# Kernel optimization log

Measured on AMD Instinct MI355X. Metric: run time of the kernel, lower is better.

## Reference

```python
import jax, jax.numpy as jnp
import numpy as np
import math

D = 256      # d_model == channels
H = 8        # nhead
DEP = D // H # depth = 32
FF = 1024    # dim_feedforward
P = 81       # 9x9 shogi board tokens
EPS = 1e-5


def setup_inputs() -> dict:
    key = jax.random.key(0)
    ks = jax.random.split(key, 8)
    B = 2048
    x = jax.random.normal(ks[0], (B, D, 9, 9), dtype=jnp.float32)
    s = 0.02
    return {
        "x": x,
        "qkv_w": jax.random.normal(ks[1], (3 * D, D // H), dtype=jnp.float32) * s,  # grouped 1x1 conv weight
        "rel_w1": jax.random.normal(ks[2], (32, D * P), dtype=jnp.float32) * s,
        "rel_w2": jax.random.normal(ks[3], (DEP * P, 32), dtype=jnp.float32) * s,
        "o_w": jax.random.normal(ks[4], (D, D), dtype=jnp.float32) * s,
        "ff_w1": jax.random.normal(ks[5], (FF, D), dtype=jnp.float32) * s,
        "ff_w2": jax.random.normal(ks[6], (D, FF), dtype=jnp.float32) * s,
        "bn1_g": jnp.ones((D,), jnp.float32),
        "bn1_b": jnp.zeros((D,), jnp.float32),
        "bn2_g": jnp.ones((D,), jnp.float32),
        "bn2_b": jnp.zeros((D,), jnp.float32),
    }


def _batchnorm(x, g, b):
    # training-mode BN: per-channel batch stats over (B, H, W), biased variance
    mean = jnp.mean(x, axis=(0, 2, 3), keepdims=True)
    var = jnp.var(x, axis=(0, 2, 3), keepdims=True)
    return (x - mean) * jax.lax.rsqrt(var + EPS) * g[None, :, None, None] + b[None, :, None, None]


def reference(x, qkv_w, rel_w1, rel_w2, o_w, ff_w1, ff_w2, bn1_g, bn1_b, bn2_g, bn2_b):
    B = x.shape[0]
    # grouped 1x1 conv QKV: group g maps its D//H input channels to 3*DEP outputs
    xg = x.reshape(B, H, D // H, P)                      # [B, H, D/H, 81]
    wg = qkv_w.reshape(H, 3 * DEP, D // H)               # [H, 3*DEP, D/H]
    qkv = jnp.einsum('goi,bgip->bgop', wg, xg).reshape(B, 3 * D, P)
    q = qkv[:, :D].reshape(B, H, DEP, P).transpose(0, 1, 3, 2)       # [B,H,81,DEP]
    k = qkv[:, D:2 * D].reshape(B, H, DEP, P)                        # [B,H,DEP,81]
    v = qkv[:, 2 * D:].reshape(B, H, DEP, P).transpose(0, 1, 3, 2)   # [B,H,81,DEP]
    # learned relative-position bias from the whole board state
    r = (x.reshape(B, -1) @ rel_w1.T) @ rel_w2.T          # [B, DEP*81]
    r = r.reshape(B, 1, DEP, P)                           # broadcast over heads
    scores = (q @ k + q @ r) / math.sqrt(DEP)             # [B,H,81,81]
    aw = jax.nn.softmax(scores, axis=-1)
    att = (aw @ v).transpose(0, 1, 3, 2).reshape(B, D, 9, 9)
    att = jnp.einsum('oc,bchw->bohw', o_w, att)           # 1x1 output projection
    x1 = _batchnorm(att + x, bn1_g, bn1_b)
    ff = jax.nn.gelu(jnp.einsum('fc,bchw->bfhw', ff_w1, x1), approximate=False)
    ff = jnp.einsum('cf,bfhw->bchw', ff_w2, ff)
    return _batchnorm(ff + x1, bn2_g, bn2_b)
```

## Files before the change

kernel.cpp:

```cpp
#include <hip/hip_runtime.h>
#include <math.h>

#define B_   2048
#define D_   256
#define H_   8
#define DEP_ 32
#define P_   81
#define FF_  1024
#define CHW  (D_*P_)
#define NPOS (B_*P_)
#define KREL (D_*P_)
#define NTOT (B_*CHW)
#define EPS_ 1e-5f
#define YTP  264
#define YTSZ (96*YTP)

typedef __attribute__((ext_vector_type(8))) short short8v;
typedef __attribute__((ext_vector_type(4))) short short4v;
typedef __attribute__((ext_vector_type(4))) float f32x4;

__device__ __forceinline__ float bf2f(unsigned short u){
    return __uint_as_float(((unsigned int)u) << 16);
}
__device__ __forceinline__ unsigned short f2bf(float f){
    unsigned int x = __float_as_uint(f);
    return (unsigned short)((x + 0x7FFFu + ((x >> 16) & 1u)) >> 16);
}
__device__ __forceinline__ float fast_gelu(float x){
    float s = __builtin_amdgcn_rcpf(1.f + __expf(-1.702f * x));
    return x * s;
}
__device__ __forceinline__ float wave16_red(float v){
    v += __shfl_xor(v, 1); v += __shfl_xor(v, 2);
    v += __shfl_xor(v, 4); v += __shfl_xor(v, 8);
    return v;
}
__device__ __forceinline__ short8v frag_redist(const f32x4 c0, const f32x4 c1, int lr, int lh){
    short8v o;
    #pragma unroll
    for (int j = 0; j < 8; ++j){
        int src = lr + 16 * (2 * (lh & 1) + (j >> 2));
        float v0 = __shfl(c0[j & 3], src);
        float v1 = __shfl(c1[j & 3], src);
        o[j] = (short)f2bf(lh < 2 ? v0 : v1);
    }
    return o;
}

__global__ __launch_bounds__(256) void k_prep(const float* __restrict__ relw1,
                                              const float* __restrict__ ffw2,
                                              const float* __restrict__ qkvw,
                                              const float* __restrict__ ow,
                                              unsigned short* __restrict__ w1rel,
                                              unsigned short* __restrict__ w2bf,
                                              unsigned short* __restrict__ qkvwb,
                                              unsigned short* __restrict__ owb){
    int i = blockIdx.x * 256 + threadIdx.x;
    int st = gridDim.x * 256;
    for (; i < 1015808; i += st){
        if (i < 663552)                w1rel[i]           = f2bf(relw1[i]);
        else if (i < 925696)           w2bf[i - 663552]   = f2bf(ffw2[i - 663552]);
        else if (i < 950272)           qkvwb[i - 925696]  = f2bf(qkvw[i - 925696]);
        else                           owb[i - 950272]    = f2bf(ow[i - 950272]);
    }
}

__global__ __launch_bounds__(256) void k_h_mfma(const float* __restrict__ x,
                                                const unsigned short* __restrict__ w1b,
                                                float* __restrict__ ph){
    const int bt = blockIdx.x >> 2, ks = blockIdx.x & 3;
    const int t = threadIdx.x, w = t >> 6, lane = t & 63;
    const int lr = lane & 15, lh = lane >> 4;
    const int b0 = bt * 16;
    f32x4 acc0 = {0.f,0.f,0.f,0.f}, acc1 = {0.f,0.f,0.f,0.f};
    const float* xrow = x + (size_t)(b0 + lr) * KREL;
    const unsigned short* wr0 = w1b + (size_t)lr * KREL;
    const unsigned short* wr1 = w1b + (size_t)(16 + lr) * KREL;
    for (int kk = w; kk < 162; kk += 4){
        const int k0 = (ks * 162 + kk) * 32 + lh * 8;
        short8v a0 = *(const short8v*)(wr0 + k0);
        short8v a1 = *(const short8v*)(wr1 + k0);
        const float4 xv0 = *(const float4*)(xrow + k0);
        const float4 xv1 = *(const float4*)(xrow + k0 + 4);
        short8v bb;
        bb[0] = (short)f2bf(xv0.x); bb[1] = (short)f2bf(xv0.y);
        bb[2] = (short)f2bf(xv0.z); bb[3] = (short)f2bf(xv0.w);
        bb[4] = (short)f2bf(xv1.x); bb[5] = (short)f2bf(xv1.y);
        bb[6] = (short)f2bf(xv1.z); bb[7] = (short)f2bf(xv1.w);
        acc0 = __builtin_amdgcn_mfma_f32_16x16x32_bf16(a0, bb, acc0, 0, 0, 0);
        acc1 = __builtin_amdgcn_mfma_f32_16x16x32_bf16(a1, bb, acc1, 0, 0, 0);
    }
    __shared__ float red[4][32][17];
    #pragma unroll
    for (int r = 0; r < 4; ++r){
        red[w][lh * 4 + r][lr]      = acc0[r];
        red[w][16 + lh * 4 + r][lr] = acc1[r];
    }
    __syncthreads();
    for (int i = t; i < 512; i += 256){
        int j = i >> 4, bb2 = i & 15;
        float s = red[0][j][bb2] + red[1][j][bb2] + red[2][j][bb2] + red[3][j][bb2];
        ph[(size_t)ks * 65536 + (size_t)(b0 + bb2) * 32 + j] = s;
    }
}

__global__ __launch_bounds__(256) void k_h_red(const float* __restrict__ ph,
                                               float* __restrict__ h){
    int i = blockIdx.x * 256 + threadIdx.x;
    h[i] = ph[i] + ph[65536 + i] + ph[131072 + i] + ph[196608 + i];
}

__global__ __launch_bounds__(512, 2) void k_attn_oproj8(const float* __restrict__ x,
                                                        const unsigned short* __restrict__ qkvwb,
                                                        const float* __restrict__ relw2,
                                                        const float* __restrict__ h,
                                                        const unsigned short* __restrict__ owb,
                                                        unsigned short* __restrict__ yT,
                                                        float* __restrict__ p1){
    const int b = blockIdx.x, t = threadIdx.x;
    const int lane = t & 63, w = t >> 6;
    const int lr = lane & 15, lh = lane >> 4;

    __shared__ __align__(16) unsigned short x1s[96 * 264];
    __shared__ __align__(16) unsigned short Rl[96 * 40];
    __shared__ __align__(16) unsigned short vL[8][32 * 104];
    __shared__ __align__(16) unsigned short pL[8][16 * 104];
    unsigned short* attT = (unsigned short*)vL;

    const float* xb = x + (size_t)b * CHW;

    {
        const float* hb = h + b * 32;
        float hreg[32];
        #pragma unroll
        for (int j = 0; j < 32; ++j) hreg[j] = hb[j];
        for (int idx = t; idx < 2592; idx += 512){
            int d = idx / 81, p = idx - d * 81;
            const float4* wr = (const float4*)(relw2 + (size_t)idx * 32);
            float s = 0.f;
            #pragma unroll
            for (int j = 0; j < 8; ++j){
                float4 wv = wr[j];
                s += wv.x * hreg[4*j] + wv.y * hreg[4*j+1] + wv.z * hreg[4*j+2] + wv.w * hreg[4*j+3];
            }
            Rl[p * 40 + d] = f2bf(s);
        }
        for (int idx = t; idx < 15 * 32; idx += 512){
            int p = 81 + (idx >> 5), d = idx & 31;
            Rl[p * 40 + d] = 0;
        }
    }
    for (int idx = t; idx < 15 * 132; idx += 512){
        int r = idx / 132, c = idx - r * 132;
        *(unsigned int*)&x1s[(81 + r) * 264 + 2 * c] = 0;
    }
    for (int idx = t; idx < 81 * 128; idx += 512){
        int c2 = idx / 81, p = idx - c2 * 81;
        int c = 2 * c2;
        unsigned int pk = (unsigned int)f2bf(xb[c * 81 + p])
                        | ((unsigned int)f2bf(xb[(c + 1) * 81 + p]) << 16);
        *(unsigned int*)&x1s[p * 264 + c] = pk;
    }
    __syncthreads();

    const int hh = w;
    const int qrow = hh * 32, krow = 256 + hh * 32, vrow = 512 + hh * 32;
    const int gq = (qrow / 96) * 32, gk = (krow / 96) * 32, gv = (vrow / 96) * 32;
    unsigned short* v_ = vL[w];
    unsigned short* p_ = pL[w];

    __builtin_amdgcn_s_setprio(1);
    short8v bqf[6];
    {
        short8v a0 = *(const short8v*)(qkvwb + (size_t)(qrow + lr) * 32 + lh * 8);
        short8v a1 = *(const short8v*)(qkvwb + (size_t)(qrow + 16 + lr) * 32 + lh * 8);
        #pragma unroll
        for (int nt = 0; nt < 6; ++nt){
            short8v bb = *(const short8v*)(x1s + (nt * 16 + lr) * 264 + gq + lh * 8);
            f32x4 c0 = {0.f,0.f,0.f,0.f}, c1 = {0.f,0.f,0.f,0.f};
            c0 = __builtin_amdgcn_mfma_f32_16x16x32_bf16(a0, bb, c0, 0, 0, 0);
            c1 = __builtin_amdgcn_mfma_f32_16x16x32_bf16(a1, bb, c1, 0, 0, 0);
            bqf[nt] = frag_redist(c0, c1, lr, lh);
        }
    }
    short8v akf[6];
    {
        short8v a0 = *(const short8v*)(qkvwb + (size_t)(krow + lr) * 32 + lh * 8);
        short8v a1 = *(const short8v*)(qkvwb + (size_t)(krow + 16 + lr) * 32 + lh * 8);
        #pragma unroll
        for (int mt = 0; mt < 6; ++mt){
            int p = mt * 16 + lr;
            short4v r0 = *(const short4v*)(Rl + p * 40 + lh * 4);
            short4v r1 = *(const short4v*)(Rl + p * 40 + 16 + lh * 4);
            f32x4 c0, c1;
            #pragma unroll
            for (int r = 0; r < 4; ++r){
                c0[r] = bf2f((unsigned short)r0[r]);
                c1[r] = bf2f((unsigned short)r1[r]);
            }
            short8v bb = *(const short8v*)(x1s + p * 264 + gk + lh * 8);
            c0 = __builtin_amdgcn_mfma_f32_16x16x32_bf16(a0, bb, c0, 0, 0, 0);
            c1 = __builtin_amdgcn_mfma_f32_16x16x32_bf16(a1, bb, c1, 0, 0, 0);
            akf[mt] = frag_redist(c0, c1, lr, lh);
        }
    }
    {
        short8v a0 = *(const short8v*)(qkvwb + (size_t)(vrow + lr) * 32 + lh * 8);
        short8v a1 = *(const short8v*)(qkvwb + (size_t)(vrow + 16 + lr) * 32 + lh * 8);
        #pragma unroll
        for (int nt = 0; nt < 6; ++nt){
            short8v bb = *(const short8v*)(x1s + (nt * 16 + lr) * 264 + gv + lh * 8);
            f32x4 c0 = {0.f,0.f,0.f,0.f}, c1 = {0.f,0.f,0.f,0.f};
            c0 = __builtin_amdgcn_mfma_f32_16x16x32_bf16(a0, bb, c0, 0, 0, 0);
            c1 = __builtin_amdgcn_mfma_f32_16x16x32_bf16(a1, bb, c1, 0, 0, 0);
            int pk = nt * 16 + lr;
            #pragma unroll
            for (int r = 0; r < 4; ++r){
                v_[(lh * 4 + r) * 104 + pk]      = f2bf(c0[r]);
                v_[(16 + lh * 4 + r) * 104 + pk] = f2bf(c1[r]);
            }
        }
    }

    f32x4 oA[6], oB[6];
    #pragma unroll
    for (int nt = 0; nt < 6; ++nt){
        f32x4 sc[6];
        #pragma unroll
        for (int mt = 0; mt < 6; ++mt){
            f32x4 z = {0.f,0.f,0.f,0.f};
            sc[mt] = __builtin_amdgcn_mfma_f32_16x16x32_bf16(akf[mt], bqf[nt], z, 0, 0, 0);
        }
        sc[5][0] = (lh == 0) ? sc[5][0] : -1e30f;
        sc[5][1] = -1e30f; sc[5][2] = -1e30f; sc[5][3] = -1e30f;
        float mx = -1e30f;
        #pragma unroll
        for (int mt = 0; mt < 6; ++mt)
        #pragma unroll
        for (int r = 0; r < 4; ++r) mx = fmaxf(mx, sc[mt][r]);
        mx = fmaxf(mx, __shfl_xor(mx, 16));
        mx = fmaxf(mx, __shfl_xor(mx, 32));
        const float scl = 0.17677669529663687f;
        float sum = 0.f;
        #pragma unroll
        for (int mt = 0; mt < 6; ++mt)
        #pragma unroll
        for (int r = 0; r < 4; ++r){
            float e = __expf((sc[mt][r] - mx) * scl);
            sc[mt][r] = e; sum += e;
        }
        sum += __shfl_xor(sum, 16);
        sum += __shfl_xor(sum, 32);
        float inv = 1.f / sum;
        #pragma unroll
        for (int mt = 0; mt < 6; ++mt){
            short4v pv;
            #pragma unroll
            for (int r = 0; r < 4; ++r) pv[r] = (short)f2bf(sc[mt][r] * inv);
            *(short4v*)(p_ + lr * 104 + mt * 16 + lh * 4) = pv;
        }
        f32x4 o0 = {0.f,0.f,0.f,0.f}, o1 = {0.f,0.f,0.f,0.f};
        #pragma unroll
        for (int ks = 0; ks < 3; ++ks){
            short8v ap  = *(const short8v*)(p_ + lr * 104 + ks * 32 + lh * 8);
            short8v bv0 = *(const short8v*)(v_ + lr * 104 + ks * 32 + lh * 8);
            short8v bv1 = *(const short8v*)(v_ + (16 + lr) * 104 + ks * 32 + lh * 8);
            o0 = __builtin_amdgcn_mfma_f32_16x16x32_bf16(ap, bv0, o0, 0, 0, 0);
            o1 = __builtin_amdgcn_mfma_f32_16x16x32_bf16(ap, bv1, o1, 0, 0, 0);
        }
        oA[nt] = o0;
        oB[nt] = o1;
    }
    __builtin_amdgcn_s_setprio(0);

    __syncthreads();
    #pragma unroll
    for (int nt = 0; nt < 6; ++nt){
        #pragma unroll
        for (int r = 0; r < 4; ++r){
            int pq = nt * 16 + lh * 4 + r;
            if (pq < 81){
                attT[pq * 264 + hh * 32 + lr]      = f2bf(oA[nt][r]);
                attT[pq * 264 + hh * 32 + 16 + lr] = f2bf(oB[nt][r]);
            } else {
                attT[pq * 264 + hh * 32 + lr]      = 0;
                attT[pq * 264 + hh * 32 + 16 + lr] = 0;
            }
        }
    }
    __syncthreads();

    const int cw = w * 32;
    f32x4 acc[2][6];
    #pragma unroll
    for (int ci = 0; ci < 2; ++ci)
    #pragma unroll
    for (int pj = 0; pj < 6; ++pj)
        acc[ci][pj] = (f32x4){0.f, 0.f, 0.f, 0.f};

    __builtin_amdgcn_s_setprio(1);
    for (int ks = 0; ks < 8; ++ks){
        const int k0 = ks * 32 + lh * 8;
        short8v a[2];
        #pragma unroll
        for (int ci = 0; ci < 2; ++ci)
            a[ci] = *(const short8v*)(owb + (size_t)(cw + ci * 16 + lr) * 256 + k0);
        #pragma unroll
        for (int pj = 0; pj < 6; ++pj){
            short8v bb = *(const short8v*)(attT + (pj * 16 + lr) * 264 + k0);
            #pragma unroll
            for (int ci = 0; ci < 2; ++ci)
                acc[ci][pj] = __builtin_amdgcn_mfma_f32_16x16x32_bf16(a[ci], bb, acc[ci][pj], 0, 0, 0);
        }
    }
    __builtin_amdgcn_s_setprio(0);
    unsigned short* yb = yT + (size_t)b * YTSZ;
    float cs[8], cq[8];
    #pragma unroll
    for (int i = 0; i < 8; ++i){ cs[i] = 0.f; cq[i] = 0.f; }
    #pragma unroll
    for (int ci = 0; ci < 2; ++ci)
    #pragma unroll
    for (int pj = 0; pj < 6; ++pj){
        int p = pj * 16 + lr;
        int c = cw + ci * 16 + lh * 4;
        short4v pk;
        if (p < 81){
            short4v xv = *(const short4v*)&x1s[p * 264 + c];
            #pragma unroll
            for (int r = 0; r < 4; ++r){
                float y = acc[ci][pj][r] + bf2f((unsigned short)xv[r]);
                pk[r] = (short)f2bf(y);
                cs[ci * 4 + r] += y;
                cq[ci * 4 + r] += y * y;
            }
        } else {
            #pragma unroll
            for (int r = 0; r < 4; ++r) pk[r] = 0;
        }
        *(short4v*)(yb + p * YTP + c) = pk;
    }
    #pragma unroll
    for (int i = 0; i < 8; ++i){
        cs[i] = wave16_red(cs[i]);
        cq[i] = wave16_red(cq[i]);
    }
    if (lr == 0){
        #pragma unroll
        for (int ci = 0; ci < 2; ++ci)
        #pragma unroll
        for (int r = 0; r < 4; ++r){
            int c = cw + ci * 16 + lh * 4 + r;
            p1[(size_t)c * 2048 + b]         = cs[ci * 4 + r];
            p1[(size_t)(256 + c) * 2048 + b] = cq[ci * 4 + r];
        }
    }
}

__global__ __launch_bounds__(256) void k_red(const float* __restrict__ part,
                                             const float* __restrict__ g, const float* __restrict__ bia,
                                             float* __restrict__ sOut, float* __restrict__ tOut){
    const int c = blockIdx.x, t = threadIdx.x;
    float s = 0.f, q = 0.f;
    #pragma unroll
    for (int i = 0; i < 8; ++i){
        s += part[(size_t)c * 2048 + t + i * 256];
        q += part[(size_t)(256 + c) * 2048 + t + i * 256];
    }
    __shared__ float rs[256], rq[256];
    rs[t] = s; rq[t] = q;
    __syncthreads();
    for (int k = 128; k; k >>= 1){
        if (t < k){ rs[t] += rs[t + k]; rq[t] += rq[t + k]; }
        __syncthreads();
    }
    if (t == 0){
        float m = rs[0] / (float)NPOS;
        float var = rq[0] / (float)NPOS - m * m;
        float sc = g[c] * rsqrtf(var + EPS_);
        sOut[c] = sc;
        tOut[c] = bia[c] - m * sc;
    }
}

__global__ __launch_bounds__(256) void k_w1prep(const float* __restrict__ w1,
                                                const float* __restrict__ s1v,
                                                const float* __restrict__ t1v,
                                                unsigned short* __restrict__ w1s,
                                                float* __restrict__ bias1){
    const int f = blockIdx.x, t = threadIdx.x;
    float wv = w1[f * 256 + t];
    w1s[f * 256 + t] = f2bf(wv * s1v[t]);
    float s = wv * t1v[t];
    #pragma unroll
    for (int m = 1; m < 64; m <<= 1) s += __shfl_xor(s, m);
    __shared__ float red[4];
    if ((t & 63) == 0) red[t >> 6] = s;
    __syncthreads();
    if (t == 0) bias1[f] = red[0] + red[1] + red[2] + red[3];
}

__global__ __launch_bounds__(256, 2) void k_ff_v4(unsigned short* __restrict__ yT,
                                                  const unsigned short* __restrict__ w1s,
                                                  const unsigned short* __restrict__ w2bf,
                                                  const float* __restrict__ bias1,
                                                  const float* __restrict__ s1, const float* __restrict__ t1,
                                                  float* __restrict__ p2){
    const int b = blockIdx.x, t = threadIdx.x;
    const int lane = t & 63, w = t >> 6;
    const int lr = lane & 15, lh = lane >> 4;

    __shared__ __align__(16) unsigned short x1s[96 * 264];
    __shared__ __align__(16) unsigned short ffs[2][96 * 72];

    {
        const short8v* src = (const short8v*)(yT + (size_t)b * YTSZ);
        short8v* dst = (short8v*)x1s;
        for (int idx = t; idx < 3168; idx += 256) dst[idx] = src[idx];
    }
    __syncthreads();

    const int cw = w * 64;
    const int fl = w * 16 + lh * 4;
    f32x4 acc2[4][6];
    #pragma unroll
    for (int ci = 0; ci < 4; ++ci)
    #pragma unroll
    for (int pj = 0; pj < 6; ++pj)
        acc2[ci][pj] = (f32x4){0.f, 0.f, 0.f, 0.f};

    auto g1_kloop = [&](int fc, f32x4 (&acc1)[6]){
        const int fbase = fc * 64 + w * 16;
        float b4[4];
        #pragma unroll
        for (int r = 0; r < 4; ++r) b4[r] = bias1[fbase + lh * 4 + r];
        #pragma unroll
        for (int pj = 0; pj < 6; ++pj){
            acc1[pj][0] = b4[0]; acc1[pj][1] = b4[1];
            acc1[pj][2] = b4[2]; acc1[pj][3] = b4[3];
        }
        __builtin_amdgcn_s_setprio(1);
        #pragma unroll
        for (int ks = 0; ks < 8; ++ks){
            const int k0 = ks * 32 + lh * 8;
            short8v a0 = *(const short8v*)(w1s + (size_t)(fbase + lr) * 256 + k0);
            #pragma unroll
            for (int pj = 0; pj < 6; ++pj){
                short8v bb = *(const short8v*)(x1s + (pj * 16 + lr) * 264 + k0);
                acc1[pj] = __builtin_amdgcn_mfma_f32_16x16x32_bf16(a0, bb, acc1[pj], 0, 0, 0);
            }
        }
        __builtin_amdgcn_s_setprio(0);
    };
    auto g2 = [&](int fc, int bf){
        __builtin_amdgcn_s_setprio(1);
        #pragma unroll
        for (int ks2 = 0; ks2 < 2; ++ks2){
            const int k0 = ks2 * 32 + lh * 8;
            short8v a2[4];
            #pragma unroll
            for (int ci = 0; ci < 4; ++ci)
                a2[ci] = *(const short8v*)(w2bf + (size_t)(cw + ci * 16 + lr) * 1024 + fc * 64 + k0);
            #pragma unroll
            for (int pj = 0; pj < 6; ++pj){
                short8v bb = *(const short8v*)(ffs[bf] + (pj * 16 + lr) * 72 + k0);
                #pragma unroll
                for (int ci = 0; ci < 4; ++ci)
                    acc2[ci][pj] = __builtin_amdgcn_mfma_f32_16x16x32_bf16(a2[ci], bb, acc2[ci][pj], 0, 0, 0);
            }
        }
        __builtin_amdgcn_s_setprio(0);
    };
    auto gelu_store = [&](const f32x4 (&acc1)[6], int bf){
        #pragma unroll
        for (int pj = 0; pj < 6; ++pj){
            int p = pj * 16 + lr;
            short4v pk;
            #pragma unroll
            for (int r = 0; r < 4; ++r)
                pk[r] = (short)f2bf(fast_gelu(acc1[pj][r]));
            *(short4v*)&ffs[bf][p * 72 + fl] = pk;
        }
    };

    {
        f32x4 acc1[6];
        g1_kloop(0, acc1);
        gelu_store(acc1, 0);
    }
    __syncthreads();
    for (int fc = 0; fc < 15; ++fc){
        f32x4 acc1[6];
        g1_kloop(fc + 1, acc1);
        g2(fc, fc & 1);
        gelu_store(acc1, (fc + 1) & 1);
        __syncthreads();
    }
    g2(15, 1);

    float sv[16], tv[16];
    #pragma unroll
    for (int ci = 0; ci < 4; ++ci)
    #pragma unroll
    for (int r = 0; r < 4; ++r){
        int c = cw + ci * 16 + lh * 4 + r;
        sv[ci * 4 + r] = s1[c];
        tv[ci * 4 + r] = t1[c];
    }
    unsigned short* zb = yT + (size_t)b * YTSZ;
    float cs[16], cq[16];
    #pragma unroll
    for (int i = 0; i < 16; ++i){ cs[i] = 0.f; cq[i] = 0.f; }
    #pragma unroll
    for (int ci = 0; ci < 4; ++ci)
    #pragma unroll
    for (int pj = 0; pj < 6; ++pj){
        int p = pj * 16 + lr;
        if (p < 81){
            int c = cw + ci * 16 + lh * 4;
            short4v yv = *(const short4v*)&x1s[p * 264 + c];
            short4v pk;
            #pragma unroll
            for (int r = 0; r < 4; ++r){
                float x1 = fmaf(bf2f((unsigned short)yv[r]), sv[ci * 4 + r], tv[ci * 4 + r]);
                float z = acc2[ci][pj][r] + x1;
                pk[r] = (short)f2bf(z);
                cs[ci * 4 + r] += z;
                cq[ci * 4 + r] += z * z;
            }
            *(short4v*)(zb + p * YTP + c) = pk;
        }
    }
    #pragma unroll
    for (int i = 0; i < 16; ++i){
        cs[i] = wave16_red(cs[i]);
        cq[i] = wave16_red(cq[i]);
    }
    if (lr == 0){
        #pragma unroll
        for (int ci = 0; ci < 4; ++ci)
        #pragma unroll
        for (int r = 0; r < 4; ++r){
            int c = cw + ci * 16 + lh * 4 + r;
            p2[(size_t)c * 2048 + b]         = cs[ci * 4 + r];
            p2[(size_t)(256 + c) * 2048 + b] = cq[ci * 4 + r];
        }
    }
}

__global__ __launch_bounds__(256) void k_bnapply_t(const unsigned short* __restrict__ yTz,
                                                   const float* __restrict__ s2, const float* __restrict__ t2,
                                                   float* __restrict__ out){
    const int b = blockIdx.x, t = threadIdx.x;
    __shared__ __align__(16) unsigned short zs[96 * 264];
    __shared__ float s2s[256], t2s[256];
    s2s[t] = s2[t];
    t2s[t] = t2[t];
    {
        const short8v* src = (const short8v*)(yTz + (size_t)b * YTSZ);
        short8v* dst = (short8v*)zs;
        for (int idx = t; idx < 3168; idx += 256) dst[idx] = src[idx];
    }
    __syncthreads();
    float* ob = out + (size_t)b * CHW;
    for (int idx = t; idx < CHW; idx += 256){
        int c = idx / 81, p = idx - c * 81;
        ob[idx] = fmaf(bf2f(zs[p * 264 + c]), s2s[c], t2s[c]);
    }
}

extern "C" void kernel_launch(void* const* d_in, const int* in_sizes, int n_in,
                              void* d_out, int out_size, void* d_ws, size_t ws_size,
                              hipStream_t stream){
    const float* x     = (const float*)d_in[0];
    const float* qkvw  = (const float*)d_in[1];
    const float* relw1 = (const float*)d_in[2];
    const float* relw2 = (const float*)d_in[3];
    const float* ow    = (const float*)d_in[4];
    const float* ffw1  = (const float*)d_in[5];
    const float* ffw2  = (const float*)d_in[6];
    const float* g1    = (const float*)d_in[7];
    const float* b1    = (const float*)d_in[8];
    const float* g2    = (const float*)d_in[9];
    const float* b2    = (const float*)d_in[10];
    float* out = (float*)d_out;
    char* ws = (char*)d_ws;

    unsigned short* w1rel = (unsigned short*)ws;
    float* h     = (float*)(ws + 1327104);
    unsigned short* w2bf  = (unsigned short*)(ws + 2117632);
    unsigned short* qkvwb = (unsigned short*)(ws + 2641920);
    unsigned short* owb   = (unsigned short*)(ws + 2691072);
    unsigned short* w1s   = (unsigned short*)(ws + 2822144);
    float* bias1 = (float*)(ws + 3346432);
    float* s1    = (float*)(ws + 3350528);
    float* t1    = (float*)(ws + 3351552);
    float* s2    = (float*)(ws + 3352576);
    float* t2    = (float*)(ws + 3353600);
    float* p1    = (float*)(ws + 3354624);
    float* p2    = (float*)(ws + 7548928);
    unsigned short* yT = (unsigned short*)(ws + 11743232);
    float* p_h = p1;

    hipLaunchKernelGGL(k_prep, dim3(1024), dim3(256), 0, stream,
                       relw1, ffw2, qkvw, ow, w1rel, w2bf, qkvwb, owb);
    hipLaunchKernelGGL(k_h_mfma, dim3(512), dim3(256), 0, stream, x, w1rel, p_h);
    hipLaunchKernelGGL(k_h_red,  dim3(256), dim3(256), 0, stream, p_h, h);
    hipLaunchKernelGGL(k_attn_oproj8, dim3(2048), dim3(512), 0, stream, x, qkvwb, relw2, h, owb, yT, p1);
    hipLaunchKernelGGL(k_red,     dim3(256),  dim3(256), 0, stream, p1, g1, b1, s1, t1);
    hipLaunchKernelGGL(k_w1prep,  dim3(1024), dim3(256), 0, stream, ffw1, s1, t1, w1s, bias1);
    hipLaunchKernelGGL(k_ff_v4,   dim3(2048), dim3(256), 0, stream, yT, w1s, w2bf, bias1, s1, t1, p2);
    hipLaunchKernelGGL(k_red,     dim3(256),  dim3(256), 0, stream, p2, g2, b2, s2, t2);
    hipLaunchKernelGGL(k_bnapply_t, dim3(2048), dim3(256), 0, stream, yT, s2, t2, out);
}
```

Before: 690.8 us.

## Switch FFN kernel to 32x32x16 MFMA tiles with larger F chunks

Rewrites the fused FFN kernel to use 32x32x16 bf16 MFMA instructions instead of 16x16x32, processing 128-wide F chunks (8 iterations instead of 16). The double-buffered software pipeline between GEMM1 and GEMM2 is replaced by a single buffer with two barriers per chunk. The intent is to cut instruction count and operand loads per FLOP and reduce the number of synchronisation rounds, at the cost of losing overlap between GELU/GEMM1 and GEMM2. Padding rows 81..95 are now computed in 32-row tiles, which adds wasted work.

```diff
diff --git a/kernel.cpp b/kernel.cpp
--- a/kernel.cpp
+++ b/kernel.cpp
@@ -18,6 +18,7 @@
 typedef __attribute__((ext_vector_type(8))) short short8v;
 typedef __attribute__((ext_vector_type(4))) short short4v;
 typedef __attribute__((ext_vector_type(4))) float f32x4;
+typedef __attribute__((ext_vector_type(16))) float f32x16;
 
 __device__ __forceinline__ float bf2f(unsigned short u){
     return __uint_as_float(((unsigned int)u) << 16);
@@ -33,6 +34,12 @@
 __device__ __forceinline__ float wave16_red(float v){
     v += __shfl_xor(v, 1); v += __shfl_xor(v, 2);
     v += __shfl_xor(v, 4); v += __shfl_xor(v, 8);
+    return v;
+}
+__device__ __forceinline__ float wave32_red(float v){
+    v += __shfl_xor(v, 1); v += __shfl_xor(v, 2);
+    v += __shfl_xor(v, 4); v += __shfl_xor(v, 8);
+    v += __shfl_xor(v, 16);
     return v;
 }
 __device__ __forceinline__ short8v frag_redist(const f32x4 c0, const f32x4 c1, int lr, int lh){
@@ -400,7 +407,7 @@
     if (t == 0) bias1[f] = red[0] + red[1] + red[2] + red[3];
 }
 
-__global__ __launch_bounds__(256, 2) void k_ff_v4(unsigned short* __restrict__ yT,
+__global__ __launch_bounds__(256, 2) void k_ff_v6(unsigned short* __restrict__ yT,
                                                   const unsigned short* __restrict__ w1s,
                                                   const unsigned short* __restrict__ w2bf,
                                                   const float* __restrict__ bias1,
@@ -408,10 +415,10 @@
                                                   float* __restrict__ p2){
     const int b = blockIdx.x, t = threadIdx.x;
     const int lane = t & 63, w = t >> 6;
-    const int lr = lane & 15, lh = lane >> 4;
+    const int lc = lane & 31, hi = lane >> 5;
 
     __shared__ __align__(16) unsigned short x1s[96 * 264];
-    __shared__ __align__(16) unsigned short ffs[2][96 * 72];
+    __shared__ __align__(16) unsigned short ffs[96 * 136];
 
     {
         const short8v* src = (const short8v*)(yT + (size_t)b * YTSZ);
@@ -421,129 +428,125 @@
     __syncthreads();
 
     const int cw = w * 64;
-    const int fl = w * 16 + lh * 4;
-    f32x4 acc2[4][6];
-    #pragma unroll
-    for (int ci = 0; ci < 4; ++ci)
-    #pragma unroll
-    for (int pj = 0; pj < 6; ++pj)
-        acc2[ci][pj] = (f32x4){0.f, 0.f, 0.f, 0.f};
-
-    auto g1_kloop = [&](int fc, f32x4 (&acc1)[6]){
-        const int fbase = fc * 64 + w * 16;
-        float b4[4];
-        #pragma unroll
-        for (int r = 0; r < 4; ++r) b4[r] = bias1[fbase + lh * 4 + r];
-        #pragma unroll
-        for (int pj = 0; pj < 6; ++pj){
-            acc1[pj][0] = b4[0]; acc1[pj][1] = b4[1];
-            acc1[pj][2] = b4[2]; acc1[pj][3] = b4[3];
+    f32x16 acc2[2][3];
+    #pragma unroll
+    for (int ct = 0; ct < 2; ++ct)
+    #pragma unroll
+    for (int pt = 0; pt < 3; ++pt)
+    #pragma unroll
+    for (int i = 0; i < 16; ++i)
+        acc2[ct][pt][i] = 0.f;
+
+    for (int fc = 0; fc < 8; ++fc){
+        const int fbase = fc * 128 + w * 32;
+        f32x16 acc1[3];
+        {
+            float bv[16];
+            #pragma unroll
+            for (int q = 0; q < 4; ++q)
+            #pragma unroll
+            for (int r = 0; r < 4; ++r)
+                bv[q * 4 + r] = bias1[fbase + 8 * q + 4 * hi + r];
+            #pragma unroll
+            for (int pt = 0; pt < 3; ++pt)
+            #pragma unroll
+            for (int i = 0; i < 16; ++i)
+                acc1[pt][i] = bv[i];
         }
         __builtin_amdgcn_s_setprio(1);
         #pragma unroll
+        for (int ks = 0; ks < 16; ++ks){
+            const int k0 = ks * 16 + hi * 8;
+            short8v a0 = *(const short8v*)(w1s + (size_t)(fbase + lc) * 256 + k0);
+            #pragma unroll
+            for (int pt = 0; pt < 3; ++pt){
+                short8v bb = *(const short8v*)(x1s + (pt * 32 + lc) * 264 + k0);
+                acc1[pt] = __builtin_amdgcn_mfma_f32_32x32x16_bf16(a0, bb, acc1[pt], 0, 0, 0);
+            }
+        }
+        __builtin_amdgcn_s_setprio(0);
+        #pragma unroll
+        for (int pt = 0; pt < 3; ++pt){
+            int p = pt * 32 + lc;
+            #pragma unroll
+            for (int q = 0; q < 4; ++q){
+                short4v pk;
+                #pragma unroll
+                for (int r = 0; r < 4; ++r)
+                    pk[r] = (short)f2bf(fast_gelu(acc1[pt][q * 4 + r]));
+                *(short4v*)&ffs[p * 136 + w * 32 + 8 * q + 4 * hi] = pk;
+            }
+        }
+        __syncthreads();
+        __builtin_amdgcn_s_setprio(1);
+        #pragma unroll
         for (int ks = 0; ks < 8; ++ks){
-            const int k0 = ks * 32 + lh * 8;
-            short8v a0 = *(const short8v*)(w1s + (size_t)(fbase + lr) * 256 + k0);
-            #pragma unroll
-            for (int pj = 0; pj < 6; ++pj){
-                short8v bb = *(const short8v*)(x1s + (pj * 16 + lr) * 264 + k0);
-                acc1[pj] = __builtin_amdgcn_mfma_f32_16x16x32_bf16(a0, bb, acc1[pj], 0, 0, 0);
+            const int kf = ks * 16 + hi * 8;
+            short8v a[2];
+            #pragma unroll
+            for (int ct = 0; ct < 2; ++ct)
+                a[ct] = *(const short8v*)(w2bf + (size_t)(cw + ct * 32 + lc) * 1024 + fc * 128 + kf);
+            #pragma unroll
+            for (int pt = 0; pt < 3; ++pt){
+                short8v bb = *(const short8v*)(ffs + (pt * 32 + lc) * 136 + kf);
+                #pragma unroll
+                for (int ct = 0; ct < 2; ++ct)
+                    acc2[ct][pt] = __builtin_amdgcn_mfma_f32_32x32x16_bf16(a[ct], bb, acc2[ct][pt], 0, 0, 0);
             }
         }
         __builtin_amdgcn_s_setprio(0);
-    };
-    auto g2 = [&](int fc, int bf){
-        __builtin_amdgcn_s_setprio(1);
-        #pragma unroll
-        for (int ks2 = 0; ks2 < 2; ++ks2){
-            const int k0 = ks2 * 32 + lh * 8;
-            short8v a2[4];
-            #pragma unroll
-            for (int ci = 0; ci < 4; ++ci)
-                a2[ci] = *(const short8v*)(w2bf + (size_t)(cw + ci * 16 + lr) * 1024 + fc * 64 + k0);
-            #pragma unroll
-            for (int pj = 0; pj < 6; ++pj){
-                short8v bb = *(const short8v*)(ffs[bf] + (pj * 16 + lr) * 72 + k0);
+        __syncthreads();
+    }
+    unsigned short* zb = yT + (size_t)b * YTSZ;
+    #pragma unroll
+    for (int ct = 0; ct < 2; ++ct){
+        float sv[16], tv[16];
+        #pragma unroll
+        for (int q = 0; q < 4; ++q)
+        #pragma unroll
+        for (int r = 0; r < 4; ++r){
+            int c = cw + ct * 32 + 8 * q + 4 * hi + r;
+            sv[q * 4 + r] = s1[c];
+            tv[q * 4 + r] = t1[c];
+        }
+        float cs[16], cq[16];
+        #pragma unroll
+        for (int i = 0; i < 16; ++i){ cs[i] = 0.f; cq[i] = 0.f; }
+        #pragma unroll
+        for (int pt = 0; pt < 3; ++pt){
+            int p = pt * 32 + lc;
+            if (p < 81){
                 #pragma unroll
-                for (int ci = 0; ci < 4; ++ci)
-                    acc2[ci][pj] = __builtin_amdgcn_mfma_f32_16x16x32_bf16(a2[ci], bb, acc2[ci][pj], 0, 0, 0);
-            }
-        }
-        __builtin_amdgcn_s_setprio(0);
-    };
-    auto gelu_store = [&](const f32x4 (&acc1)[6], int bf){
-        #pragma unroll
-        for (int pj = 0; pj < 6; ++pj){
-            int p = pj * 16 + lr;
-            short4v pk;
-            #pragma unroll
-            for (int r = 0; r < 4; ++r)
-                pk[r] = (short)f2bf(fast_gelu(acc1[pj][r]));
-            *(short4v*)&ffs[bf][p * 72 + fl] = pk;
-        }
-    };
-
-    {
-        f32x4 acc1[6];
-        g1_kloop(0, acc1);
-        gelu_store(acc1, 0);
-    }
-    __syncthreads();
-    for (int fc = 0; fc < 15; ++fc){
-        f32x4 acc1[6];
-        g1_kloop(fc + 1, acc1);
-        g2(fc, fc & 1);
-        gelu_store(acc1, (fc + 1) & 1);
-        __syncthreads();
-    }
-    g2(15, 1);
-
-    float sv[16], tv[16];
-    #pragma unroll
-    for (int ci = 0; ci < 4; ++ci)
-    #pragma unroll
-    for (int r = 0; r < 4; ++r){
-        int c = cw + ci * 16 + lh * 4 + r;
-        sv[ci * 4 + r] = s1[c];
-        tv[ci * 4 + r] = t1[c];
-    }
-    unsigned short* zb = yT + (size_t)b * YTSZ;
-    float cs[16], cq[16];
-    #pragma unroll
-    for (int i = 0; i < 16; ++i){ cs[i] = 0.f; cq[i] = 0.f; }
-    #pragma unroll
-    for (int ci = 0; ci < 4; ++ci)
-    #pragma unroll
-    for (int pj = 0; pj < 6; ++pj){
-        int p = pj * 16 + lr;
-        if (p < 81){
-            int c = cw + ci * 16 + lh * 4;
-            short4v yv = *(const short4v*)&x1s[p * 264 + c];
-            short4v pk;
+                for (int q = 0; q < 4; ++q){
+                    int c = cw + ct * 32 + 8 * q + 4 * hi;
+                    short4v yv = *(const short4v*)&x1s[p * 264 + c];
+                    short4v pk;
+                    #pragma unroll
+                    for (int r = 0; r < 4; ++r){
+                        float x1 = fmaf(bf2f((unsigned short)yv[r]), sv[q * 4 + r], tv[q * 4 + r]);
+                        float z = acc2[ct][pt][q * 4 + r] + x1;
+                        pk[r] = (short)f2bf(z);
+                        cs[q * 4 + r] += z;
+                        cq[q * 4 + r] += z * z;
+                    }
+                    *(short4v*)(zb + p * YTP + c) = pk;
+                }
+            }
+        }
+        #pragma unroll
+        for (int i = 0; i < 16; ++i){
+            cs[i] = wave32_red(cs[i]);
+            cq[i] = wave32_red(cq[i]);
+        }
+        if (lc == 0){
+            #pragma unroll
+            for (int q = 0; q < 4; ++q)
             #pragma unroll
             for (int r = 0; r < 4; ++r){
-                float x1 = fmaf(bf2f((unsigned short)yv[r]), sv[ci * 4 + r], tv[ci * 4 + r]);
-                float z = acc2[ci][pj][r] + x1;
-                pk[r] = (short)f2bf(z);
-                cs[ci * 4 + r] += z;
-                cq[ci * 4 + r] += z * z;
-            }
-            *(short4v*)(zb + p * YTP + c) = pk;
-        }
-    }
-    #pragma unroll
-    for (int i = 0; i < 16; ++i){
-        cs[i] = wave16_red(cs[i]);
-        cq[i] = wave16_red(cq[i]);
-    }
-    if (lr == 0){
-        #pragma unroll
-        for (int ci = 0; ci < 4; ++ci)
-        #pragma unroll
-        for (int r = 0; r < 4; ++r){
-            int c = cw + ci * 16 + lh * 4 + r;
-            p2[(size_t)c * 2048 + b]         = cs[ci * 4 + r];
-            p2[(size_t)(256 + c) * 2048 + b] = cq[ci * 4 + r];
+                int c = cw + ct * 32 + 8 * q + 4 * hi + r;
+                p2[(size_t)c * 2048 + b]         = cs[q * 4 + r];
+                p2[(size_t)(256 + c) * 2048 + b] = cq[q * 4 + r];
+            }
         }
     }
 }
@@ -609,7 +612,7 @@
     hipLaunchKernelGGL(k_attn_oproj8, dim3(2048), dim3(512), 0, stream, x, qkvwb, relw2, h, owb, yT, p1);
     hipLaunchKernelGGL(k_red,     dim3(256),  dim3(256), 0, stream, p1, g1, b1, s1, t1);
     hipLaunchKernelGGL(k_w1prep,  dim3(1024), dim3(256), 0, stream, ffw1, s1, t1, w1s, bias1);
-    hipLaunchKernelGGL(k_ff_v4,   dim3(2048), dim3(256), 0, stream, yT, w1s, w2bf, bias1, s1, t1, p2);
+    hipLaunchKernelGGL(k_ff_v6,   dim3(2048), dim3(256), 0, stream, yT, w1s, w2bf, bias1, s1, t1, p2);
     hipLaunchKernelGGL(k_red,     dim3(256),  dim3(256), 0, stream, p2, g2, b2, s2, t2);
     hipLaunchKernelGGL(k_bnapply_t, dim3(2048), dim3(256), 0, stream, yT, s2, t2, out);
 }
```

Result: slower. 704.7 us (+2.0%).

## Retile FF kernel waves as 2x2 over features and positions

Applied to the files above, without the earlier changes.

Splits the four waves of the feed-forward kernel into a 2x2 grid, with two halves over features/channels and two halves over positions, instead of each wave owning one feature/channel slice across all positions. Each wave now loads two W1 fragments per k-step and eight W2 fragments per chunk, and reuses each activation fragment across more MFMAs, which changes the balance of LDS reads to global weight reads. Because two position halves now produce partial BN statistics for the same channels, they are written to two buffers (reusing p1 as the second) and summed by a new k_red2. This raises accumulator register pressure (acc2 is 8x3), which may threaten the two-blocks-per-SIMD occupancy target.

```diff
diff --git a/kernel.cpp b/kernel.cpp
--- a/kernel.cpp
+++ b/kernel.cpp
@@ -383,6 +383,35 @@
     }
 }
 
+__global__ __launch_bounds__(256) void k_red2(const float* __restrict__ pa,
+                                              const float* __restrict__ pb,
+                                              const float* __restrict__ g, const float* __restrict__ bia,
+                                              float* __restrict__ sOut, float* __restrict__ tOut){
+    const int c = blockIdx.x, t = threadIdx.x;
+    float s = 0.f, q = 0.f;
+    #pragma unroll
+    for (int i = 0; i < 8; ++i){
+        size_t idx = (size_t)c * 2048 + t + i * 256;
+        size_t idq = (size_t)(256 + c) * 2048 + t + i * 256;
+        s += pa[idx] + pb[idx];
+        q += pa[idq] + pb[idq];
+    }
+    __shared__ float rs[256], rq[256];
+    rs[t] = s; rq[t] = q;
+    __syncthreads();
+    for (int k = 128; k; k >>= 1){
+        if (t < k){ rs[t] += rs[t + k]; rq[t] += rq[t + k]; }
+        __syncthreads();
+    }
+    if (t == 0){
+        float m = rs[0] / (float)NPOS;
+        float var = rq[0] / (float)NPOS - m * m;
+        float sc = g[c] * rsqrtf(var + EPS_);
+        sOut[c] = sc;
+        tOut[c] = bia[c] - m * sc;
+    }
+}
+
 __global__ __launch_bounds__(256) void k_w1prep(const float* __restrict__ w1,
                                                 const float* __restrict__ s1v,
                                                 const float* __restrict__ t1v,
@@ -400,15 +429,18 @@
     if (t == 0) bias1[f] = red[0] + red[1] + red[2] + red[3];
 }
 
-__global__ __launch_bounds__(256, 2) void k_ff_v4(unsigned short* __restrict__ yT,
+__global__ __launch_bounds__(256, 2) void k_ff_v9(unsigned short* __restrict__ yT,
                                                   const unsigned short* __restrict__ w1s,
                                                   const unsigned short* __restrict__ w2bf,
                                                   const float* __restrict__ bias1,
                                                   const float* __restrict__ s1, const float* __restrict__ t1,
-                                                  float* __restrict__ p2){
+                                                  float* __restrict__ p2a,
+                                                  float* __restrict__ p2b){
     const int b = blockIdx.x, t = threadIdx.x;
     const int lane = t & 63, w = t >> 6;
     const int lr = lane & 15, lh = lane >> 4;
+    const int wf = w & 1, wp = w >> 1;
+    const int p0 = wp * 48;
 
     __shared__ __align__(16) unsigned short x1s[96 * 264];
     __shared__ __align__(16) unsigned short ffs[2][96 * 72];
@@ -420,34 +452,39 @@
     }
     __syncthreads();
 
-    const int cw = w * 64;
-    const int fl = w * 16 + lh * 4;
-    f32x4 acc2[4][6];
-    #pragma unroll
-    for (int ci = 0; ci < 4; ++ci)
-    #pragma unroll
-    for (int pj = 0; pj < 6; ++pj)
+    f32x4 acc2[8][3];
+    #pragma unroll
+    for (int ci = 0; ci < 8; ++ci)
+    #pragma unroll
+    for (int pj = 0; pj < 3; ++pj)
         acc2[ci][pj] = (f32x4){0.f, 0.f, 0.f, 0.f};
 
-    auto g1_kloop = [&](int fc, f32x4 (&acc1)[6]){
-        const int fbase = fc * 64 + w * 16;
-        float b4[4];
-        #pragma unroll
-        for (int r = 0; r < 4; ++r) b4[r] = bias1[fbase + lh * 4 + r];
-        #pragma unroll
-        for (int pj = 0; pj < 6; ++pj){
-            acc1[pj][0] = b4[0]; acc1[pj][1] = b4[1];
-            acc1[pj][2] = b4[2]; acc1[pj][3] = b4[3];
+    auto g1_kloop = [&](int fc, f32x4 (&acc1)[2][3]){
+        const int fbase = fc * 64 + wf * 32;
+        float b4[2][4];
+        #pragma unroll
+        for (int fi = 0; fi < 2; ++fi)
+        #pragma unroll
+        for (int r = 0; r < 4; ++r)
+            b4[fi][r] = bias1[fbase + fi * 16 + lh * 4 + r];
+        #pragma unroll
+        for (int fi = 0; fi < 2; ++fi)
+        #pragma unroll
+        for (int pj = 0; pj < 3; ++pj){
+            acc1[fi][pj][0] = b4[fi][0]; acc1[fi][pj][1] = b4[fi][1];
+            acc1[fi][pj][2] = b4[fi][2]; acc1[fi][pj][3] = b4[fi][3];
         }
         __builtin_amdgcn_s_setprio(1);
         #pragma unroll
         for (int ks = 0; ks < 8; ++ks){
             const int k0 = ks * 32 + lh * 8;
             short8v a0 = *(const short8v*)(w1s + (size_t)(fbase + lr) * 256 + k0);
-            #pragma unroll
-            for (int pj = 0; pj < 6; ++pj){
-                short8v bb = *(const short8v*)(x1s + (pj * 16 + lr) * 264 + k0);
-                acc1[pj] = __builtin_amdgcn_mfma_f32_16x16x32_bf16(a0, bb, acc1[pj], 0, 0, 0);
+            short8v a1 = *(const short8v*)(w1s + (size_t)(fbase + 16 + lr) * 256 + k0);
+            #pragma unroll
+            for (int pj = 0; pj < 3; ++pj){
+                short8v bb = *(const short8v*)(x1s + (p0 + pj * 16 + lr) * 264 + k0);
+                acc1[0][pj] = __builtin_amdgcn_mfma_f32_16x16x32_bf16(a0, bb, acc1[0][pj], 0, 0, 0);
+                acc1[1][pj] = __builtin_amdgcn_mfma_f32_16x16x32_bf16(a1, bb, acc1[1][pj], 0, 0, 0);
             }
         }
         __builtin_amdgcn_s_setprio(0);
@@ -457,40 +494,43 @@
         #pragma unroll
         for (int ks2 = 0; ks2 < 2; ++ks2){
             const int k0 = ks2 * 32 + lh * 8;
-            short8v a2[4];
-            #pragma unroll
-            for (int ci = 0; ci < 4; ++ci)
-                a2[ci] = *(const short8v*)(w2bf + (size_t)(cw + ci * 16 + lr) * 1024 + fc * 64 + k0);
-            #pragma unroll
-            for (int pj = 0; pj < 6; ++pj){
-                short8v bb = *(const short8v*)(ffs[bf] + (pj * 16 + lr) * 72 + k0);
+            short8v a2[8];
+            #pragma unroll
+            for (int ci = 0; ci < 8; ++ci)
+                a2[ci] = *(const short8v*)(w2bf + (size_t)(wf * 128 + ci * 16 + lr) * 1024 + fc * 64 + k0);
+            #pragma unroll
+            for (int pj = 0; pj < 3; ++pj){
+                short8v bb = *(const short8v*)(ffs[bf] + (p0 + pj * 16 + lr) * 72 + k0);
                 #pragma unroll
-                for (int ci = 0; ci < 4; ++ci)
+                for (int ci = 0; ci < 8; ++ci)
                     acc2[ci][pj] = __builtin_amdgcn_mfma_f32_16x16x32_bf16(a2[ci], bb, acc2[ci][pj], 0, 0, 0);
             }
         }
         __builtin_amdgcn_s_setprio(0);
     };
-    auto gelu_store = [&](const f32x4 (&acc1)[6], int bf){
-        #pragma unroll
-        for (int pj = 0; pj < 6; ++pj){
-            int p = pj * 16 + lr;
+    auto gelu_store = [&](const f32x4 (&acc1)[2][3], int bf){
+        #pragma unroll
+        for (int fi = 0; fi < 2; ++fi)
+        #pragma unroll
+        for (int pj = 0; pj < 3; ++pj){
+            int p = p0 + pj * 16 + lr;
+            int fl = wf * 32 + fi * 16 + lh * 4;
             short4v pk;
             #pragma unroll
             for (int r = 0; r < 4; ++r)
-                pk[r] = (short)f2bf(fast_gelu(acc1[pj][r]));
+                pk[r] = (short)f2bf(fast_gelu(acc1[fi][pj][r]));
             *(short4v*)&ffs[bf][p * 72 + fl] = pk;
         }
     };
 
     {
-        f32x4 acc1[6];
+        f32x4 acc1[2][3];
         g1_kloop(0, acc1);
         gelu_store(acc1, 0);
     }
     __syncthreads();
     for (int fc = 0; fc < 15; ++fc){
-        f32x4 acc1[6];
+        f32x4 acc1[2][3];
         g1_kloop(fc + 1, acc1);
         g2(fc, fc & 1);
         gelu_store(acc1, (fc + 1) & 1);
@@ -498,52 +538,43 @@
     }
     g2(15, 1);
 
-    float sv[16], tv[16];
-    #pragma unroll
-    for (int ci = 0; ci < 4; ++ci)
-    #pragma unroll
-    for (int r = 0; r < 4; ++r){
-        int c = cw + ci * 16 + lh * 4 + r;
-        sv[ci * 4 + r] = s1[c];
-        tv[ci * 4 + r] = t1[c];
-    }
     unsigned short* zb = yT + (size_t)b * YTSZ;
-    float cs[16], cq[16];
-    #pragma unroll
-    for (int i = 0; i < 16; ++i){ cs[i] = 0.f; cq[i] = 0.f; }
-    #pragma unroll
-    for (int ci = 0; ci < 4; ++ci)
-    #pragma unroll
-    for (int pj = 0; pj < 6; ++pj){
-        int p = pj * 16 + lr;
-        if (p < 81){
-            int c = cw + ci * 16 + lh * 4;
-            short4v yv = *(const short4v*)&x1s[p * 264 + c];
-            short4v pk;
+    float* pout = wp ? p2b : p2a;
+    #pragma unroll
+    for (int ci = 0; ci < 8; ++ci){
+        const int c = wf * 128 + ci * 16 + lh * 4;
+        float sv4[4], tv4[4];
+        #pragma unroll
+        for (int r = 0; r < 4; ++r){ sv4[r] = s1[c + r]; tv4[r] = t1[c + r]; }
+        float cs4[4] = {0.f,0.f,0.f,0.f}, cq4[4] = {0.f,0.f,0.f,0.f};
+        #pragma unroll
+        for (int pj = 0; pj < 3; ++pj){
+            int p = p0 + pj * 16 + lr;
+            if (p < 81){
+                short4v yv = *(const short4v*)&x1s[p * 264 + c];
+                short4v pk;
+                #pragma unroll
+                for (int r = 0; r < 4; ++r){
+                    float x1 = fmaf(bf2f((unsigned short)yv[r]), sv4[r], tv4[r]);
+                    float z = acc2[ci][pj][r] + x1;
+                    pk[r] = (short)f2bf(z);
+                    cs4[r] += z;
+                    cq4[r] += z * z;
+                }
+                *(short4v*)(zb + p * YTP + c) = pk;
+            }
+        }
+        #pragma unroll
+        for (int r = 0; r < 4; ++r){
+            cs4[r] = wave16_red(cs4[r]);
+            cq4[r] = wave16_red(cq4[r]);
+        }
+        if (lr == 0){
             #pragma unroll
             for (int r = 0; r < 4; ++r){
-                float x1 = fmaf(bf2f((unsigned short)yv[r]), sv[ci * 4 + r], tv[ci * 4 + r]);
-                float z = acc2[ci][pj][r] + x1;
-                pk[r] = (short)f2bf(z);
-                cs[ci * 4 + r] += z;
-                cq[ci * 4 + r] += z * z;
-            }
-            *(short4v*)(zb + p * YTP + c) = pk;
-        }
-    }
-    #pragma unroll
-    for (int i = 0; i < 16; ++i){
-        cs[i] = wave16_red(cs[i]);
-        cq[i] = wave16_red(cq[i]);
-    }
-    if (lr == 0){
-        #pragma unroll
-        for (int ci = 0; ci < 4; ++ci)
-        #pragma unroll
-        for (int r = 0; r < 4; ++r){
-            int c = cw + ci * 16 + lh * 4 + r;
-            p2[(size_t)c * 2048 + b]         = cs[ci * 4 + r];
-            p2[(size_t)(256 + c) * 2048 + b] = cq[ci * 4 + r];
+                pout[(size_t)(c + r) * 2048 + b]         = cs4[r];
+                pout[(size_t)(256 + c + r) * 2048 + b]   = cq4[r];
+            }
         }
     }
 }
@@ -581,8 +612,8 @@
     const float* ffw2  = (const float*)d_in[6];
     const float* g1    = (const float*)d_in[7];
     const float* b1    = (const float*)d_in[8];
-    const float* g2    = (const float*)d_in[9];
-    const float* b2    = (const float*)d_in[10];
+    const float* g2v   = (const float*)d_in[9];
+    const float* b2v   = (const float*)d_in[10];
     float* out = (float*)d_out;
     char* ws = (char*)d_ws;
 
@@ -609,7 +640,7 @@
     hipLaunchKernelGGL(k_attn_oproj8, dim3(2048), dim3(512), 0, stream, x, qkvwb, relw2, h, owb, yT, p1);
     hipLaunchKernelGGL(k_red,     dim3(256),  dim3(256), 0, stream, p1, g1, b1, s1, t1);
     hipLaunchKernelGGL(k_w1prep,  dim3(1024), dim3(256), 0, stream, ffw1, s1, t1, w1s, bias1);
-    hipLaunchKernelGGL(k_ff_v4,   dim3(2048), dim3(256), 0, stream, yT, w1s, w2bf, bias1, s1, t1, p2);
-    hipLaunchKernelGGL(k_red,     dim3(256),  dim3(256), 0, stream, p2, g2, b2, s2, t2);
+    hipLaunchKernelGGL(k_ff_v9,   dim3(2048), dim3(256), 0, stream, yT, w1s, w2bf, bias1, s1, t1, p2, p1);
+    hipLaunchKernelGGL(k_red2,    dim3(256),  dim3(256), 0, stream, p2, p1, g2v, b2v, s2, t2);
     hipLaunchKernelGGL(k_bnapply_t, dim3(2048), dim3(256), 0, stream, yT, s2, t2, out);
 }
```

Result: slower. 914.7 us (+32.4%).
